# Performance work log

Measured on AMD Instinct MI355X. Metric: run time of the kernel, lower is better.

The kernel has to match this reference:

```python
import jax, jax.numpy as jnp
import numpy as np

B, N, D, H = 64, 197, 768, 12
HD = D // H          # 64
MLP = 4 * D          # 3072
WIN = 14
NUM_REL = (2 * WIN - 1) * (2 * WIN - 1) + 3  # 732
SCALE = HD ** -0.5
DCF_SCALE = 1.0
EPS = 1e-5


def _make_rel_index(wh, ww):
    coords = np.stack(np.meshgrid(np.arange(wh), np.arange(ww), indexing='ij'))  # [2, wh, ww]
    flat = coords.reshape(2, -1)
    rel = flat[:, :, None] - flat[:, None, :]          # [2, L, L]
    rel = rel.transpose(1, 2, 0).astype(np.int64)      # [L, L, 2]
    rel[..., 0] += wh - 1
    rel[..., 1] += ww - 1
    rel[..., 0] *= 2 * ww - 1
    idx = np.zeros((wh * ww + 1, wh * ww + 1), dtype=np.int32)
    idx[1:, 1:] = rel.sum(-1)
    nrd = (2 * wh - 1) * (2 * ww - 1) + 3
    idx[0, :] = nrd - 3
    idx[:, 0] = nrd - 2
    idx[0, 0] = nrd - 1
    return idx


def _ln(x, w, b):
    m = x.mean(-1, keepdims=True)
    v = ((x - m) ** 2).mean(-1, keepdims=True)
    return (x - m) * jax.lax.rsqrt(v + EPS) * w + b


def setup_inputs() -> dict:
    key = jax.random.key(0)
    ks = jax.random.split(key, 32)
    rnd = lambda i, shp, s=0.02: jax.random.normal(ks[i], shp, jnp.float32) * s
    return {
        'x': jax.random.normal(ks[0], (B, N, D), jnp.float32),
        'w_qkv': rnd(1, (3 * D, D)),
        'q_bias': rnd(2, (D,)),
        'v_bias': rnd(3, (D,)),
        'ssf_scale_qkv': 1.0 + rnd(4, (3 * D,)),
        'ssf_shift_qkv': rnd(5, (3 * D,)),
        'rel_bias_table': rnd(6, (NUM_REL, H)),
        'bases_coeff': rnd(7, (H, H)),
        'w_proj': rnd(8, (D, D)),
        'b_proj': rnd(9, (D,)),
        'ssf_scale_proj': 1.0 + rnd(10, (D,)),
        'ssf_shift_proj': rnd(11, (D,)),
        'norm1_w': jnp.ones((D,), jnp.float32),
        'norm1_b': jnp.zeros((D,), jnp.float32),
        'norm2_w': jnp.ones((D,), jnp.float32),
        'norm2_b': jnp.zeros((D,), jnp.float32),
        'ssf_scale_1': 1.0 + rnd(12, (D,)),
        'ssf_shift_1': rnd(13, (D,)),
        'ssf_scale_2': 1.0 + rnd(14, (D,)),
        'ssf_shift_2': rnd(15, (D,)),
        'w_fc1': rnd(16, (MLP, D)),
        'b_fc1': rnd(17, (MLP,)),
        'w_fc2': rnd(18, (D, MLP)),
        'b_fc2': rnd(19, (D,)),
        'ssf_scale_mlp': 1.0 + rnd(20, (D,)),
        'ssf_shift_mlp': rnd(21, (D,)),
        'gamma_1': jnp.full((D,), 0.1, jnp.float32),
        'gamma_2': jnp.full((D,), 0.1, jnp.float32),
        'rel_pos_index': jnp.asarray(_make_rel_index(WIN, WIN)),
    }


def reference(x, w_qkv, q_bias, v_bias, ssf_scale_qkv, ssf_shift_qkv,
              rel_bias_table, bases_coeff, w_proj, b_proj,
              ssf_scale_proj, ssf_shift_proj, norm1_w, norm1_b, norm2_w, norm2_b,
              ssf_scale_1, ssf_shift_1, ssf_scale_2, ssf_shift_2,
              w_fc1, b_fc1, w_fc2, b_fc2, ssf_scale_mlp, ssf_shift_mlp,
              gamma_1, gamma_2, rel_pos_index):
    # --- attention branch (eval mode: all dropouts are identity) ---
    h = _ln(x, norm1_w, norm1_b) * ssf_scale_1 + ssf_shift_1
    qkv_bias = jnp.concatenate([q_bias, jnp.zeros_like(v_bias), v_bias])
    qkv = h @ w_qkv.T + qkv_bias                       # [B, N, 3D]
    qkv = qkv * ssf_scale_qkv + ssf_shift_qkv
    qkv = qkv.reshape(B, N, 3, H, HD).transpose(2, 0, 3, 1, 4)  # [3, B, H, N, hd]
    q, k, v = qkv[0] * SCALE, qkv[1], qkv[2]
    attn = jnp.einsum('bhnd,bhmd->bhnm', q, k)         # [B, H, N, N]
    bias = rel_bias_table[rel_pos_index.reshape(-1)].reshape(N, N, H).transpose(2, 0, 1)
    attn = jax.nn.softmax(attn + bias[None], axis=-1)
    # dcf head mixing
    coeff = bases_coeff.T * DCF_SCALE + jnp.eye(H, dtype=attn.dtype)
    attn = jnp.einsum('bhnl,hk->bknl', attn, coeff)
    y = jnp.einsum('bhnm,bhmd->bnhd', attn, v).reshape(B, N, D)
    y = y @ w_proj.T + b_proj
    y = y * ssf_scale_proj + ssf_shift_proj
    x = x + gamma_1 * y
    # --- MLP branch ---
    h = _ln(x, norm2_w, norm2_b) * ssf_scale_2 + ssf_shift_2
    m = jax.nn.gelu(h @ w_fc1.T + b_fc1, approximate=False)
    m = m @ w_fc2.T + b_fc2
    m = m * ssf_scale_mlp + ssf_shift_mlp
    return x + gamma_2 * m
```

## Files before the change

### kernel.cpp

```cpp
#include <hip/hip_runtime.h>

typedef unsigned short u16;
using f32x4  = __attribute__((ext_vector_type(4))) float;
using bf16x8 = __attribute__((ext_vector_type(8))) __bf16;

#define Bz   64
#define Nn   197
#define Dd   768
#define Hh   12
#define HDp  64
#define MLPD 3072
#define ROWS (Bz*Nn)
#define NM   (Nn*Nn)
#define NPAD 224

#define OFF_H    0UL
#define OFF_X1   19365888UL
#define OFF_BIA  58097664UL
#define OFF_WB   59960496UL
#define OFF_CH   74116272UL
#define WQKV_E 0UL
#define WPRJ_E 1769472UL
#define WFC1_E 2359296UL
#define WFC2_E 4718592UL
#define QKV_B  907776UL
#define P_B    1059072UL
#define VT_B   344064UL
#define CHUNK_B 2310912UL

__device__ inline float b2f(u16 v){ unsigned u = ((unsigned)v) << 16; float f; __builtin_memcpy(&f,&u,4); return f; }
__device__ inline u16 f2b(float f){ unsigned u; __builtin_memcpy(&u,&f,4); u += 0x7FFFu + ((u>>16)&1u); return (u16)(u>>16); }

__device__ inline float gelu_f(float x){
    float z  = fabsf(x) * 0.70710678118f;
    float t  = 1.f / (1.f + 0.3275911f * z);
    float y  = t*(0.254829592f + t*(-0.284496736f + t*(1.421413741f + t*(-1.453152027f + t*1.061405429f))));
    float er = 1.f - y * __expf(-z*z);
    er = copysignf(er, x);
    return 0.5f * x * (1.f + er);
}

__device__ inline void gload_lds16(const u16* g, u16* l) {
    __builtin_amdgcn_global_load_lds((const __attribute__((address_space(1))) void*)g,
                                     (__attribute__((address_space(3))) void*)l, 16, 0, 0);
}

__global__ __launch_bounds__(256)
void conv_b16(const float* __restrict__ src, u16* __restrict__ dst, int n4)
{
    int t = blockIdx.x*256 + threadIdx.x;
    if (t >= n4) return;
    float4 v = *(const float4*)(src + (size_t)t*4);
    u16* d = dst + (size_t)t*4;
    d[0] = f2b(v.x); d[1] = f2b(v.y); d[2] = f2b(v.z); d[3] = f2b(v.w);
}

template<int EPI>
__global__ __launch_bounds__(512, 1)
void gemm256v(const u16* __restrict__ A, const u16* __restrict__ W, void* __restrict__ Cp,
              int M, int N, int K, int lda, int ldw,
              const float* __restrict__ e0, const float* __restrict__ e1,
              const float* __restrict__ e2, const float* __restrict__ e3,
              const float* __restrict__ ef)
{
    extern __shared__ u16 lds[];
    constexpr int SWEEP = 4096;
    constexpr int ICA  = 2;
    constexpr int ICB  = 2;
    constexpr int ASZ  = 256 * 32;
    constexpr int BSZ  = 256 * 32;
    constexpr int ABUF = 2 * ASZ;
    constexpr int BBUF = 2 * BSZ;
    constexpr int MF   = 8;
    constexpr int MH   = 4;

    u16* sA = lds;
    u16* sB = lds + 2 * ABUF;

    const int tid  = threadIdx.x;
    const int lane = tid & 63;
    const int wave = tid >> 6;
    const int wr   = wave >> 2;
    const int wc   = wave & 3;
    const int rid  = lane & 15;
    const int kg   = lane >> 4;
    const int m0   = blockIdx.y * 256;
    const int n0   = blockIdx.x * 256;
    const int t8   = tid * 8;

    const u16* asrc[2][ICA]; int adst[2][ICA];
    const u16* bsrc[2][ICB]; int bdst[2][ICB];
#pragma unroll
    for (int s = 0; s < 2; ++s) {
#pragma unroll
        for (int i = 0; i < ICA; ++i) {
            int e = i*SWEEP + t8, r = e >> 5;
            int g = ((e >> 3) & 3) ^ ((r >> 1) & 3);
            int row = m0 + r; if (row > M-1) row = M-1;
            asrc[s][i] = A + (size_t)row*lda + s*32 + g*8;
            adst[s][i] = s*ASZ + e;
        }
#pragma unroll
        for (int i = 0; i < ICB; ++i) {
            int e = i*SWEEP + t8, r = e >> 5;
            int g = ((e >> 3) & 3) ^ ((r >> 1) & 3);
            int col = n0 + r; if (col > N-1) col = N-1;
            bsrc[s][i] = W + (size_t)col*ldw + s*32 + g*8;
            bdst[s][i] = s*BSZ + e;
        }
    }

    const int koA   = (kg ^ ((rid >> 1) & 3)) * 8;
    const int aRow0 = (wr*128 + rid) * 32 + koA;
    const int bRow  = (wc*64  + rid) * 32 + koA;

    f32x4 acc[MF][4];
#pragma unroll
    for (int i = 0; i < MF; ++i)
#pragma unroll
        for (int j = 0; j < 4; ++j) acc[i][j] = (f32x4){0.f,0.f,0.f,0.f};

#pragma unroll
    for (int i = 0; i < ICA; ++i) gload_lds16(asrc[0][i], sA + adst[0][i]);
#pragma unroll
    for (int i = 0; i < ICB; ++i) gload_lds16(bsrc[0][i], sB + bdst[0][i]);
    asm volatile("" ::: "memory");
#pragma unroll
    for (int i = 0; i < ICA; ++i) gload_lds16(asrc[1][i], sA + adst[1][i]);
#pragma unroll
    for (int i = 0; i < ICB; ++i) gload_lds16(bsrc[1][i], sB + bdst[1][i]);

    const int NT = K >> 6;
    for (int t = 0; t < NT; ++t) {
        const int p  = t & 1;
        const size_t kpre = (size_t)(t + 1) * 64;
        const u16* paB = sA + p * ABUF;
        const u16* pbB = sB + p * BBUF;
        const int  qa  = (p ^ 1) * ABUF;
        const int  qb  = (p ^ 1) * BBUF;
        bf16x8 af[MH], wf[4];

        asm volatile("s_waitcnt vmcnt(4) lgkmcnt(0)\n\ts_barrier" ::: "memory");
#pragma unroll
        for (int i = 0; i < ICA; ++i) gload_lds16(asrc[0][i] + kpre, sA + adst[0][i] + qa);
#pragma unroll
        for (int i = 0; i < ICB; ++i) gload_lds16(bsrc[0][i] + kpre, sB + bdst[0][i] + qb);
        asm volatile("" ::: "memory");
#pragma unroll
        for (int i = 0; i < ICA; ++i) gload_lds16(asrc[1][i] + kpre, sA + adst[1][i] + qa);
#pragma unroll
        for (int i = 0; i < ICB; ++i) gload_lds16(bsrc[1][i] + kpre, sB + bdst[1][i] + qb);

        {
            const u16* pa = paB + aRow0;
#pragma unroll
            for (int f = 0; f < MH; ++f) af[f] = *(const bf16x8*)(pa + f*512);
            const u16* pb = pbB + bRow;
#pragma unroll
            for (int j = 0; j < 4; ++j) wf[j] = *(const bf16x8*)(pb + j*512);
            __builtin_amdgcn_s_setprio(1);
#pragma unroll
            for (int f = 0; f < MH; ++f)
#pragma unroll
                for (int j = 0; j < 4; ++j)
                    acc[f][j] = __builtin_amdgcn_mfma_f32_16x16x32_bf16(af[f], wf[j], acc[f][j], 0, 0, 0);
            __builtin_amdgcn_s_setprio(0);
        }
        {
            const u16* pa = paB + aRow0 + MH*512;
#pragma unroll
            for (int f = 0; f < MH; ++f) af[f] = *(const bf16x8*)(pa + f*512);
            __builtin_amdgcn_s_setprio(1);
#pragma unroll
            for (int f = 0; f < MH; ++f)
#pragma unroll
                for (int j = 0; j < 4; ++j)
                    acc[MH+f][j] = __builtin_amdgcn_mfma_f32_16x16x32_bf16(af[f], wf[j], acc[MH+f][j], 0, 0, 0);
            __builtin_amdgcn_s_setprio(0);
        }
        asm volatile("s_waitcnt vmcnt(8) lgkmcnt(0)\n\ts_barrier" ::: "memory");
        {
            const u16* pa = paB + ASZ + aRow0;
#pragma unroll
            for (int f = 0; f < MH; ++f) af[f] = *(const bf16x8*)(pa + f*512);
            const u16* pb = pbB + BSZ + bRow;
#pragma unroll
            for (int j = 0; j < 4; ++j) wf[j] = *(const bf16x8*)(pb + j*512);
            __builtin_amdgcn_s_setprio(1);
#pragma unroll
            for (int f = 0; f < MH; ++f)
#pragma unroll
                for (int j = 0; j < 4; ++j)
                    acc[f][j] = __builtin_amdgcn_mfma_f32_16x16x32_bf16(af[f], wf[j], acc[f][j], 0, 0, 0);
            __builtin_amdgcn_s_setprio(0);
        }
        {
            const u16* pa = paB + ASZ + aRow0 + MH*512;
#pragma unroll
            for (int f = 0; f < MH; ++f) af[f] = *(const bf16x8*)(pa + f*512);
            __builtin_amdgcn_s_setprio(1);
#pragma unroll
            for (int f = 0; f < MH; ++f)
#pragma unroll
                for (int j = 0; j < 4; ++j)
                    acc[MH+f][j] = __builtin_amdgcn_mfma_f32_16x16x32_bf16(af[f], wf[j], acc[MH+f][j], 0, 0, 0);
            __builtin_amdgcn_s_setprio(0);
        }
    }
    asm volatile("s_waitcnt vmcnt(0)" ::: "memory");
    __syncthreads();

    float* ka = (float*)lds;
    float* kb = ka + 256;
    if (tid < 256) {
        int gn = n0 + tid;
        if constexpr (EPI == 0) {
            float mql = (gn < 768) ? 0.125f : 1.f;
            float bias = 0.f;
            if (gn < 768) bias = e0[gn];
            else if (gn >= 1536) bias = e1[gn-1536];
            float sc = e2[gn];
            ka[tid] = sc * mql;
            kb[tid] = (bias * sc + e3[gn]) * mql;
        } else if constexpr (EPI == 4) {
            ka[tid] = 0.f;
            kb[tid] = e0[gn];
        } else {
            float sc = e1[gn];
            ka[tid] = sc;
            kb[tid] = e0[gn]*sc + e2[gn];
        }
    }
    __syncthreads();
    const int rq = (lane >> 4) * 4;
    const int cc = lane & 15;
    float kaj[4], kbj[4];
#pragma unroll
    for (int j = 0; j < 4; ++j) {
        int c = wc*64 + j*16 + cc;
        kaj[j] = ka[c]; kbj[j] = kb[c];
    }
    __syncthreads();

    if constexpr (EPI == 0 || EPI == 4) {
        u16* ct = lds;
#pragma unroll
        for (int i = 0; i < MF; ++i) {
#pragma unroll
            for (int j = 0; j < 4; ++j) {
#pragma unroll
                for (int r = 0; r < 4; ++r) {
                    int rowL = wr*128 + i*16 + rq + r;
                    int col  = wc*64 + j*16 + cc;
                    float v = acc[i][j][r];
                    u16 o;
                    if constexpr (EPI == 0) o = f2b(v*kaj[j] + kbj[j]);
                    else                    o = f2b(gelu_f(v + kbj[j]));
                    ct[rowL*264 + col] = o;
                }
            }
        }
        __syncthreads();
        constexpr int ldc = (EPI == 0) ? 2304 : 3072;
        u16* C = (u16*)Cp;
#pragma unroll
        for (int sw = 0; sw < 16; ++sw) {
            int rowL = sw*16 + (tid >> 5);
            int gm = m0 + rowL;
            if (gm < M) {
                int col0 = (tid & 31) * 8;
                *(uint4*)(C + (size_t)gm*ldc + n0 + col0) =
                    *(const uint4*)(ct + rowL*264 + col0);
            }
        }
    } else {
        float* cf = (float*)lds;
        float* C = (float*)Cp;
#pragma unroll
        for (int h = 0; h < 2; ++h) {
            if (wr == h) {
#pragma unroll
                for (int i = 0; i < MF; ++i) {
#pragma unroll
                    for (int j = 0; j < 4; ++j) {
#pragma unroll
                        for (int r = 0; r < 4; ++r) {
                            int rowH = i*16 + rq + r;
                            int col  = wc*64 + j*16 + cc;
                            cf[rowH*260 + col] = acc[i][j][r]*kaj[j] + kbj[j];
                        }
                    }
                }
            }
            __syncthreads();
#pragma unroll
            for (int sw = 0; sw < 16; ++sw) {
                int rowH = sw*8 + (tid >> 6);
                int gm = m0 + h*128 + rowH;
                if (gm < M) {
                    int col0 = (tid & 63) * 4;
                    f32x4 v  = *(const f32x4*)(cf + rowH*260 + col0);
                    size_t gidx = (size_t)gm*768 + n0 + col0;
                    f32x4 xv = *(const f32x4*)(ef + gidx);
                    f32x4 g3 = *(const f32x4*)(e3 + n0 + col0);
                    f32x4 o;
#pragma unroll
                    for (int q = 0; q < 4; ++q) o[q] = xv[q] + g3[q]*v[q];
                    *(f32x4*)(C + gidx) = o;
                }
            }
            __syncthreads();
        }
    }
}

template<int EPI>
__global__ __launch_bounds__(256, 2)
void gemm128p(const u16* __restrict__ A, const u16* __restrict__ W, void* __restrict__ Cp,
              int M, int N, int K, int lda, int ldw,
              const float* __restrict__ e0, const float* __restrict__ e1,
              const float* __restrict__ e2, const float* __restrict__ e3,
              const float* __restrict__ e4, const float* __restrict__ ef)
{
    extern __shared__ u16 lds[];
    constexpr int SWEEP = 2048;
    constexpr int ICA  = 2;
    constexpr int ICB  = 2;
    constexpr int ASZ  = 128 * 32;
    constexpr int BSZ  = 128 * 32;
    constexpr int ABUF = 2 * ASZ;
    constexpr int BBUF = 2 * BSZ;
    constexpr int MF   = 4;
    constexpr int MH   = 2;

    u16* sA = lds;
    u16* sB = lds + 2 * ABUF;

    const int tid  = threadIdx.x;
    const int lane = tid & 63;
    const int wave = tid >> 6;
    const int wr   = wave >> 1;
    const int wc   = wave & 1;
    const int rid  = lane & 15;
    const int kg   = lane >> 4;
    const int m0   = blockIdx.y * 128;
    const int n0   = blockIdx.x * 128;
    const int t8   = tid * 8;

    const u16* asrc[2][ICA]; int adst[2][ICA];
    const u16* bsrc[2][ICB]; int bdst[2][ICB];
#pragma unroll
    for (int s = 0; s < 2; ++s) {
#pragma unroll
        for (int i = 0; i < ICA; ++i) {
            int e = i*SWEEP + t8, r = e >> 5;
            int g = ((e >> 3) & 3) ^ ((r >> 1) & 3);
            int row = m0 + r; if (row > M-1) row = M-1;
            asrc[s][i] = A + (size_t)row*lda + s*32 + g*8;
            adst[s][i] = s*ASZ + e;
        }
#pragma unroll
        for (int i = 0; i < ICB; ++i) {
            int e = i*SWEEP + t8, r = e >> 5;
            int g = ((e >> 3) & 3) ^ ((r >> 1) & 3);
            int col = n0 + r; if (col > N-1) col = N-1;
            bsrc[s][i] = W + (size_t)col*ldw + s*32 + g*8;
            bdst[s][i] = s*BSZ + e;
        }
    }

    const int koA   = (kg ^ ((rid >> 1) & 3)) * 8;
    const int aRow0 = (wr*64 + rid) * 32 + koA;
    const int bRow  = (wc*64 + rid) * 32 + koA;

    f32x4 acc[MF][4];
#pragma unroll
    for (int i = 0; i < MF; ++i)
#pragma unroll
        for (int j = 0; j < 4; ++j) acc[i][j] = (f32x4){0.f,0.f,0.f,0.f};

#pragma unroll
    for (int i = 0; i < ICA; ++i) gload_lds16(asrc[0][i], sA + adst[0][i]);
#pragma unroll
    for (int i = 0; i < ICB; ++i) gload_lds16(bsrc[0][i], sB + bdst[0][i]);
    asm volatile("" ::: "memory");
#pragma unroll
    for (int i = 0; i < ICA; ++i) gload_lds16(asrc[1][i], sA + adst[1][i]);
#pragma unroll
    for (int i = 0; i < ICB; ++i) gload_lds16(bsrc[1][i], sB + bdst[1][i]);

    const int NT = K >> 6;
    for (int t = 0; t < NT; ++t) {
        const int p  = t & 1;
        const size_t kpre = (size_t)(t + 1) * 64;
        const u16* paB = sA + p * ABUF;
        const u16* pbB = sB + p * BBUF;
        const int  qa  = (p ^ 1) * ABUF;
        const int  qb  = (p ^ 1) * BBUF;
        bf16x8 af[MH], wf[4];

        asm volatile("s_waitcnt vmcnt(4) lgkmcnt(0)\n\ts_barrier" ::: "memory");
#pragma unroll
        for (int i = 0; i < ICA; ++i) gload_lds16(asrc[0][i] + kpre, sA + adst[0][i] + qa);
#pragma unroll
        for (int i = 0; i < ICB; ++i) gload_lds16(bsrc[0][i] + kpre, sB + bdst[0][i] + qb);
        asm volatile("" ::: "memory");
#pragma unroll
        for (int i = 0; i < ICA; ++i) gload_lds16(asrc[1][i] + kpre, sA + adst[1][i] + qa);
#pragma unroll
        for (int i = 0; i < ICB; ++i) gload_lds16(bsrc[1][i] + kpre, sB + bdst[1][i] + qb);

        {
            const u16* pa = paB + aRow0;
#pragma unroll
            for (int f = 0; f < MH; ++f) af[f] = *(const bf16x8*)(pa + f*512);
            const u16* pb = pbB + bRow;
#pragma unroll
            for (int j = 0; j < 4; ++j) wf[j] = *(const bf16x8*)(pb + j*512);
            __builtin_amdgcn_s_setprio(1);
#pragma unroll
            for (int f = 0; f < MH; ++f)
#pragma unroll
                for (int j = 0; j < 4; ++j)
                    acc[f][j] = __builtin_amdgcn_mfma_f32_16x16x32_bf16(af[f], wf[j], acc[f][j], 0, 0, 0);
            __builtin_amdgcn_s_setprio(0);
        }
        {
            const u16* pa = paB + aRow0 + MH*512;
#pragma unroll
            for (int f = 0; f < MH; ++f) af[f] = *(const bf16x8*)(pa + f*512);
            __builtin_amdgcn_s_setprio(1);
#pragma unroll
            for (int f = 0; f < MH; ++f)
#pragma unroll
                for (int j = 0; j < 4; ++j)
                    acc[MH+f][j] = __builtin_amdgcn_mfma_f32_16x16x32_bf16(af[f], wf[j], acc[MH+f][j], 0, 0, 0);
            __builtin_amdgcn_s_setprio(0);
        }
        asm volatile("s_waitcnt vmcnt(8) lgkmcnt(0)\n\ts_barrier" ::: "memory");
        {
            const u16* pa = paB + ASZ + aRow0;
#pragma unroll
            for (int f = 0; f < MH; ++f) af[f] = *(const bf16x8*)(pa + f*512);
            const u16* pb = pbB + BSZ + bRow;
#pragma unroll
            for (int j = 0; j < 4; ++j) wf[j] = *(const bf16x8*)(pb + j*512);
            __builtin_amdgcn_s_setprio(1);
#pragma unroll
            for (int f = 0; f < MH; ++f)
#pragma unroll
                for (int j = 0; j < 4; ++j)
                    acc[f][j] = __builtin_amdgcn_mfma_f32_16x16x32_bf16(af[f], wf[j], acc[f][j], 0, 0, 0);
            __builtin_amdgcn_s_setprio(0);
        }
        {
            const u16* pa = paB + ASZ + aRow0 + MH*512;
#pragma unroll
            for (int f = 0; f < MH; ++f) af[f] = *(const bf16x8*)(pa + f*512);
            __builtin_amdgcn_s_setprio(1);
#pragma unroll
            for (int f = 0; f < MH; ++f)
#pragma unroll
                for (int j = 0; j < 4; ++j)
                    acc[MH+f][j] = __builtin_amdgcn_mfma_f32_16x16x32_bf16(af[f], wf[j], acc[MH+f][j], 0, 0, 0);
            __builtin_amdgcn_s_setprio(0);
        }
    }
    asm volatile("s_waitcnt vmcnt(0)" ::: "memory");
    __syncthreads();

    float* ka = (float*)lds;
    float* kb = ka + 128;
    if (tid < 128) {
        int gn = n0 + tid;
        float sc = e1[gn];
        ka[tid] = sc;
        kb[tid] = e0[gn]*sc + e2[gn];
    }
    __syncthreads();
    const int rq = (lane >> 4) * 4;
    const int cc = lane & 15;
    float kaj[4], kbj[4];
#pragma unroll
    for (int j = 0; j < 4; ++j) {
        int c = wc*64 + j*16 + cc;
        kaj[j] = ka[c]; kbj[j] = kb[c];
    }
    __syncthreads();

    float* cf = (float*)lds;
    const float* RES = e4;
    float* C = (float*)Cp;
#pragma unroll
    for (int h = 0; h < 2; ++h) {
        if (wr == h) {
#pragma unroll
            for (int i = 0; i < MF; ++i) {
#pragma unroll
                for (int j = 0; j < 4; ++j) {
#pragma unroll
                    for (int r = 0; r < 4; ++r) {
                        int rowH = i*16 + rq + r;
                        int col  = wc*64 + j*16 + cc;
                        cf[rowH*132 + col] = acc[i][j][r]*kaj[j] + kbj[j];
                    }
                }
            }
        }
        __syncthreads();
#pragma unroll
        for (int sw = 0; sw < 8; ++sw) {
            int rowH = sw*8 + (tid >> 5);
            int gm = m0 + h*64 + rowH;
            if (gm < M) {
                int col0 = (tid & 31) * 4;
                f32x4 v  = *(const f32x4*)(cf + rowH*132 + col0);
                size_t gidx = (size_t)gm*768 + n0 + col0;
                f32x4 xv = *(const f32x4*)(RES + gidx);
                f32x4 g3 = *(const f32x4*)(e3 + n0 + col0);
                f32x4 o;
#pragma unroll
                for (int q = 0; q < 4; ++q) o[q] = xv[q] + g3[q]*v[q];
                *(f32x4*)(C + gidx) = o;
            }
        }
        __syncthreads();
    }
}

template<int EPI>
__global__ __launch_bounds__(256)
void gemm_nt(const u16* __restrict__ A, const u16* __restrict__ W, void* __restrict__ Cp,
             int M, int N, int K, int lda, int ldw, int b0,
             const float* __restrict__ ef)
{
    __shared__ __align__(16) u16 csm[(EPI == 1) ? 32768 : 16384];
    const int tid  = threadIdx.x;
    const int lane = tid & 63;
    const int wave = tid >> 6;
    const int z    = blockIdx.z;
    const int m0   = wave*64;
    const int n0   = blockIdx.x*64;
    const int rid  = lane & 15;
    const int kq   = (lane >> 4) * 8;

    const u16* Ab = A;
    const u16* Wb = W;
    if constexpr (EPI == 1) {
        int bb = z/12, hh = z - bb*12;
        Ab = A + ((size_t)bb*Nn)*2304 + hh*64;
        Wb = W + ((size_t)bb*Nn)*2304 + 768 + hh*64;
    } else {
        Ab = A + (size_t)z*Nn*NPAD;
        Wb = W + (size_t)z*HDp*NPAD;
    }

    f32x4 acc[4][4];
#pragma unroll
    for (int i = 0; i < 4; ++i)
#pragma unroll
        for (int j = 0; j < 4; ++j) acc[i][j] = (f32x4){0.f,0.f,0.f,0.f};

    for (int k0 = 0; k0 < K; k0 += 32) {
        bf16x8 af[4], wf[4];
#pragma unroll
        for (int i = 0; i < 4; ++i) {
            int r = m0 + i*16 + rid; if (r > M-1) r = M-1;
            af[i] = *(const bf16x8*)(Ab + (size_t)r*lda + k0 + kq);
        }
#pragma unroll
        for (int j = 0; j < 4; ++j) {
            int c = n0 + j*16 + rid; if (c > N-1) c = N-1;
            wf[j] = *(const bf16x8*)(Wb + (size_t)c*ldw + k0 + kq);
        }
#pragma unroll
        for (int i = 0; i < 4; ++i)
#pragma unroll
            for (int j = 0; j < 4; ++j)
                acc[i][j] = __builtin_amdgcn_mfma_f32_16x16x32_bf16(af[i], wf[j], acc[i][j], 0, 0, 0);
    }

    const int rq = (lane >> 4) * 4;
    const int cc = lane & 15;

    if constexpr (EPI == 1) {
        float* cs = (float*)csm;
#pragma unroll
        for (int i = 0; i < 4; ++i)
#pragma unroll
            for (int j = 0; j < 4; ++j)
#pragma unroll
                for (int r = 0; r < 4; ++r)
                    cs[(m0 + i*16 + rq + r)*64 + j*16 + cc] = acc[i][j][r];
        __syncthreads();
        int hh = z - (z/12)*12;
        const float* bsrc = ef + (size_t)hh*NM;
        u16* P = (u16*)Cp + (size_t)z*Nn*NPAD;
        for (int sw = 0; sw < 13; ++sw) {
            int row = sw*16 + (tid >> 4);
            int col0 = (tid & 15) * 4;
            int gn = n0 + col0;
            if (row < Nn && gn < NPAD) {
                f32x4 v = *(const f32x4*)(cs + row*64 + col0);
                const float* bp = bsrc + (size_t)row*Nn + gn;
                float b0v = bp[0], b1v = bp[1], b2v = bp[2], b3v = bp[3];
                unsigned lo = (unsigned)f2b(v[0]+b0v) | ((unsigned)f2b(v[1]+b1v) << 16);
                unsigned hi = (unsigned)f2b(v[2]+b2v) | ((unsigned)f2b(v[3]+b3v) << 16);
                uint2 pk; pk.x = lo; pk.y = hi;
                *(uint2*)(P + (size_t)row*NPAD + gn) = pk;
            }
        }
    } else {
        u16* cs = csm;
#pragma unroll
        for (int i = 0; i < 4; ++i)
#pragma unroll
            for (int j = 0; j < 4; ++j)
#pragma unroll
                for (int r = 0; r < 4; ++r)
                    cs[(m0 + i*16 + rq + r)*64 + j*16 + cc] = f2b(acc[i][j][r]);
        __syncthreads();
        int bb = z/12, kk = z - bb*12;
        u16* Y = (u16*)Cp + ((size_t)(b0+bb)*Nn)*768 + kk*64;
        for (int sw = 0; sw < 7; ++sw) {
            int row = sw*32 + (tid >> 3);
            if (row < Nn) {
                int col0 = (tid & 7) * 8;
                *(uint4*)(Y + (size_t)row*768 + col0) = *(const uint4*)(cs + row*64 + col0);
            }
        }
    }
}

__global__ __launch_bounds__(256)
void ln_ssf(const float* __restrict__ x, const float* __restrict__ w, const float* __restrict__ bb,
            const float* __restrict__ sc, const float* __restrict__ sh, u16* __restrict__ out)
{
    const int row = blockIdx.x, tid = threadIdx.x;
    const float* xr = x + (size_t)row * 768;
    float v[3], s1 = 0.f, s2 = 0.f;
#pragma unroll
    for (int i = 0; i < 3; ++i) {
        float f = xr[tid + i*256];
        v[i] = f; s1 += f; s2 += f*f;
    }
    for (int o = 32; o > 0; o >>= 1) { s1 += __shfl_xor(s1, o); s2 += __shfl_xor(s2, o); }
    __shared__ float r1[4], r2[4];
    int wv = tid >> 6;
    if ((tid & 63) == 0) { r1[wv] = s1; r2[wv] = s2; }
    __syncthreads();
    s1 = r1[0]+r1[1]+r1[2]+r1[3];
    s2 = r2[0]+r2[1]+r2[2]+r2[3];
    float mean = s1 * (1.f/768.f);
    float var  = s2 * (1.f/768.f) - mean*mean;
    float rstd = rsqrtf(fmaxf(var, 0.f) + 1e-5f);
#pragma unroll
    for (int i = 0; i < 3; ++i) {
        int c = tid + i*256;
        float h = (v[i] - mean) * rstd * w[c] + bb[c];
        h = h * sc[c] + sh[c];
        out[(size_t)row*768 + c] = f2b(h);
    }
}

__global__ __launch_bounds__(256)
void bias_gather(const int* __restrict__ idx, const float* __restrict__ table, float* __restrict__ biasf)
{
    int t = blockIdx.x*256 + threadIdx.x;
    if (t >= NM) return;
    int id = idx[t];
#pragma unroll
    for (int h = 0; h < 12; ++h)
        biasf[(size_t)h*NM + t] = table[id*12 + h];
}

__global__ __launch_bounds__(256)
void softmax_dcf(u16* __restrict__ P, const float* __restrict__ bases, int nb)
{
    __shared__ float cf[144];
    int tid = threadIdx.x;
    if (tid < 144) {
        int k = tid / 12, h = tid - k*12;
        cf[h*12 + k] = bases[k*12 + h] + (h == k ? 1.f : 0.f);
    }
    __syncthreads();
    int ridx = blockIdx.x*4 + (tid >> 6);
    if (ridx >= nb*Nn) return;
    int lane = tid & 63;
    int m0 = lane * 4;
    int bb = ridx / Nn, n = ridx - bb*Nn;
    const size_t hs = (size_t)Nn*NPAD;
    u16* base = P + ((size_t)bb*12)*hs + (size_t)n*NPAD;

    float e[12][4];
#pragma unroll
    for (int h = 0; h < 12; ++h) {
        float s[4];
        if (m0 < NPAD) {
            uint2 pv = *(const uint2*)(base + h*hs + m0);
            s[0] = b2f((u16)(pv.x & 0xFFFF)); s[1] = b2f((u16)(pv.x >> 16));
            s[2] = b2f((u16)(pv.y & 0xFFFF)); s[3] = b2f((u16)(pv.y >> 16));
        } else { s[0]=s[1]=s[2]=s[3] = -1e30f; }
#pragma unroll
        for (int j = 0; j < 4; ++j) if (m0 + j >= Nn) s[j] = -1e30f;
        float mx = fmaxf(fmaxf(s[0], s[1]), fmaxf(s[2], s[3]));
        for (int o = 32; o > 0; o >>= 1) mx = fmaxf(mx, __shfl_xor(mx, o));
        float sum = 0.f;
#pragma unroll
        for (int j = 0; j < 4; ++j) {
            float ev = __expf(fmaxf(s[j] - mx, -80.f));
            if (m0 + j >= Nn) ev = 0.f;
            e[h][j] = ev; sum += ev;
        }
        for (int o = 32; o > 0; o >>= 1) sum += __shfl_xor(sum, o);
        float inv = 1.f / sum;
#pragma unroll
        for (int j = 0; j < 4; ++j) e[h][j] *= inv;
    }
    if (m0 < NPAD) {
#pragma unroll
        for (int k = 0; k < 12; ++k) {
            float o0 = 0.f, o1 = 0.f, o2 = 0.f, o3 = 0.f;
#pragma unroll
            for (int h = 0; h < 12; ++h) {
                float c = cf[h*12 + k];
                o0 += e[h][0]*c; o1 += e[h][1]*c; o2 += e[h][2]*c; o3 += e[h][3]*c;
            }
            unsigned lo = (unsigned)f2b(o0) | ((unsigned)f2b(o1) << 16);
            unsigned hi = (unsigned)f2b(o2) | ((unsigned)f2b(o3) << 16);
            uint2 pk; pk.x = lo; pk.y = hi;
            *(uint2*)(base + k*hs + m0) = pk;
        }
    }
}

__global__ __launch_bounds__(256)
void v_transpose(const u16* __restrict__ qkv, u16* __restrict__ vT)
{
    __shared__ u16 lds[64*198];
    int z = blockIdx.x;
    int bb = z/12, hh = z - bb*12;
    int tid = threadIdx.x;
    const u16* src = qkv + ((size_t)bb*Nn)*2304 + 1536 + hh*64;
    for (int e = tid; e < Nn*64; e += 256) {
        int m = e >> 6, d = e & 63;
        lds[d*198 + m] = src[(size_t)m*2304 + d];
    }
    __syncthreads();
    u16* dst = vT + (size_t)z*64*NPAD;
    for (int e = tid; e < 64*NPAD; e += 256) {
        int d = e / NPAD, m = e - d*NPAD;
        dst[e] = (m < Nn) ? lds[d*198 + m] : (u16)0;
    }
}

extern "C" void kernel_launch(void* const* d_in, const int* in_sizes, int n_in,
                              void* d_out, int out_size, void* d_ws, size_t ws_size,
                              hipStream_t stream)
{
    const float* x       = (const float*)d_in[0];
    const float* w_qkv   = (const float*)d_in[1];
    const float* q_bias  = (const float*)d_in[2];
    const float* v_bias  = (const float*)d_in[3];
    const float* s_qkv   = (const float*)d_in[4];
    const float* sh_qkv  = (const float*)d_in[5];
    const float* rel_tab = (const float*)d_in[6];
    const float* bases   = (const float*)d_in[7];
    const float* w_proj  = (const float*)d_in[8];
    const float* b_proj  = (const float*)d_in[9];
    const float* s_proj  = (const float*)d_in[10];
    const float* sh_proj = (const float*)d_in[11];
    const float* n1w     = (const float*)d_in[12];
    const float* n1b     = (const float*)d_in[13];
    const float* n2w     = (const float*)d_in[14];
    const float* n2b     = (const float*)d_in[15];
    const float* ss1     = (const float*)d_in[16];
    const float* ssh1    = (const float*)d_in[17];
    const float* ss2     = (const float*)d_in[18];
    const float* ssh2    = (const float*)d_in[19];
    const float* w_fc1   = (const float*)d_in[20];
    const float* b_fc1   = (const float*)d_in[21];
    const float* w_fc2   = (const float*)d_in[22];
    const float* b_fc2   = (const float*)d_in[23];
    const float* s_mlp   = (const float*)d_in[24];
    const float* sh_mlp  = (const float*)d_in[25];
    const float* g1      = (const float*)d_in[26];
    const float* g2      = (const float*)d_in[27];
    const int*   relidx  = (const int*)d_in[28];

    char*  ws   = (char*)d_ws;
    u16*   hbuf = (u16*)(ws + OFF_H);
    float* x1   = (float*)(ws + OFF_X1);
    float* bia  = (float*)(ws + OFF_BIA);
    u16*   wb   = (u16*)(ws + OFF_WB);
    float* out  = (float*)d_out;

    u16* wqkvB = wb + WQKV_E;
    u16* wprjB = wb + WPRJ_E;
    u16* wfc1B = wb + WFC1_E;
    u16* wfc2B = wb + WFC2_E;

    hipFuncSetAttribute(reinterpret_cast<const void*>(&gemm256v<0>),
                        hipFuncAttributeMaxDynamicSharedMemorySize, 139264);
    hipFuncSetAttribute(reinterpret_cast<const void*>(&gemm256v<4>),
                        hipFuncAttributeMaxDynamicSharedMemorySize, 139264);
    hipFuncSetAttribute(reinterpret_cast<const void*>(&gemm256v<5>),
                        hipFuncAttributeMaxDynamicSharedMemorySize, 139264);
    hipFuncSetAttribute(reinterpret_cast<const void*>(&gemm128p<3>),
                        hipFuncAttributeMaxDynamicSharedMemorySize, 65536);

    int nb = 64;
    while (nb > 1 && OFF_CH + (size_t)nb*CHUNK_B > ws_size) nb >>= 1;
    const int nchunk = 64 / nb;
    u16* qkvC = (u16*)(ws + OFF_CH);
    u16* PC   = (u16*)(ws + OFF_CH + (size_t)nb*QKV_B);
    u16* vTC  = (u16*)(ws + OFF_CH + (size_t)nb*(QKV_B + P_B));

    conv_b16<<<dim3(1728), dim3(256), 0, stream>>>(w_qkv, wqkvB, 442368);
    conv_b16<<<dim3(576),  dim3(256), 0, stream>>>(w_proj, wprjB, 147456);
    conv_b16<<<dim3(2304), dim3(256), 0, stream>>>(w_fc1, wfc1B, 589824);
    conv_b16<<<dim3(2304), dim3(256), 0, stream>>>(w_fc2, wfc2B, 589824);

    ln_ssf<<<dim3(ROWS), dim3(256), 0, stream>>>(x, n1w, n1b, ss1, ssh1, hbuf);
    bias_gather<<<dim3(152), dim3(256), 0, stream>>>(relidx, rel_tab, bia);

    for (int c = 0; c < nchunk; ++c) {
        const int b0 = c * nb;
        const int nrows = nb * Nn;
        const int gy = (nrows + 255) / 256;
        gemm256v<0><<<dim3(9, gy), dim3(512), 139264, stream>>>(
            hbuf + (size_t)b0*Nn*768, wqkvB, qkvC,
            nrows, 2304, 768, 768, 768, q_bias, v_bias, s_qkv, sh_qkv, nullptr);
        v_transpose<<<dim3(nb*12), dim3(256), 0, stream>>>(qkvC, vTC);
        gemm_nt<1><<<dim3(4, 1, nb*12), dim3(256), 0, stream>>>(
            qkvC, qkvC, PC, Nn, Nn, 64, 2304, 2304, 0, bia);
        softmax_dcf<<<dim3((nb*Nn + 3)/4), dim3(256), 0, stream>>>(PC, bases, nb);
        gemm_nt<2><<<dim3(1, 1, nb*12), dim3(256), 0, stream>>>(
            PC, vTC, hbuf, Nn, 64, NPAD, NPAD, NPAD, b0, nullptr);
    }

    gemm128p<3><<<dim3(6, 99), dim3(256), 65536, stream>>>(
        hbuf, wprjB, x1, ROWS, 768, 768, 768, 768,
        b_proj, s_proj, sh_proj, g1, x, nullptr);
    ln_ssf<<<dim3(ROWS), dim3(256), 0, stream>>>(x1, n2w, n2b, ss2, ssh2, hbuf);

    u16* mlpC = qkvC;
    size_t avail = (ws_size > OFF_CH) ? (ws_size - OFF_CH) : (size_t)CHUNK_B;
    int nrM = (int)(avail / (MLPD * 2));
    if (nrM < 1) nrM = 1;
    if (nrM > ROWS) nrM = ROWS;
    for (int r0 = 0; r0 < ROWS; r0 += nrM) {
        int cr = ROWS - r0; if (cr > nrM) cr = nrM;
        int gy = (cr + 255) / 256;
        gemm256v<4><<<dim3(12, gy), dim3(512), 139264, stream>>>(
            hbuf + (size_t)r0*768, wfc1B, mlpC, cr, 3072, 768, 768, 768,
            b_fc1, nullptr, nullptr, nullptr, nullptr);
        gemm256v<5><<<dim3(3, gy), dim3(512), 139264, stream>>>(
            mlpC, wfc2B, out + (size_t)r0*768, cr, 768, 3072, 3072, 3072,
            b_fc2, s_mlp, sh_mlp, g2, x1 + (size_t)r0*768);
    }
}
```

Before: 744.8 us.

## Generalize big GEMM to 16 waves, interleave prefetch loads with MFMA phases

Templates the 256-row GEMM on tile width and thread count, and runs QKV and FC1 with 1024 threads so each wave owns a 64x64 sub-tile instead of 128x64. FC2 now uses a 256x128 tile with 512 threads, doubling its grid width for better CU coverage. The global-to-LDS prefetches are split and interleaved between the MFMA sub-phases rather than issued all at once at the top of each iteration, with the waitcnt/barrier thresholds adjusted to match. The smaller per-wave tiles lower register use and raise the wave count per CU. The cost is less data reuse per wave and more barrier participants per block.

```diff
diff --git a/kernel.cpp b/kernel.cpp
--- a/kernel.cpp
+++ b/kernel.cpp
@@ -55,24 +55,27 @@
     d[0] = f2b(v.x); d[1] = f2b(v.y); d[2] = f2b(v.z); d[3] = f2b(v.w);
 }
 
-template<int EPI>
-__global__ __launch_bounds__(512, 1)
-void gemm256v(const u16* __restrict__ A, const u16* __restrict__ W, void* __restrict__ Cp,
-              int M, int N, int K, int lda, int ldw,
-              const float* __restrict__ e0, const float* __restrict__ e1,
-              const float* __restrict__ e2, const float* __restrict__ e3,
-              const float* __restrict__ ef)
+template<int EPI, int BN, int TH>
+__global__ __launch_bounds__(TH)
+void gemmv(const u16* __restrict__ A, const u16* __restrict__ W, void* __restrict__ Cp,
+           int M, int N, int K, int lda, int ldw,
+           const float* __restrict__ e0, const float* __restrict__ e1,
+           const float* __restrict__ e2, const float* __restrict__ e3,
+           const float* __restrict__ ef)
 {
     extern __shared__ u16 lds[];
-    constexpr int SWEEP = 4096;
-    constexpr int ICA  = 2;
-    constexpr int ICB  = 2;
-    constexpr int ASZ  = 256 * 32;
-    constexpr int BSZ  = 256 * 32;
+    constexpr int BM   = 256;
+    constexpr int SWEEP = TH * 8;
+    constexpr int ICA  = (BM * 32) / SWEEP;
+    constexpr int ICB  = (BN * 32) / SWEEP;
+    constexpr int VN   = ICA + ICB;
+    constexpr int ASZ  = BM * 32;
+    constexpr int BSZ  = BN * 32;
     constexpr int ABUF = 2 * ASZ;
     constexpr int BBUF = 2 * BSZ;
-    constexpr int MF   = 8;
-    constexpr int MH   = 4;
+    constexpr int WCN  = BN / 64;
+    constexpr int MF   = 4;
+    constexpr int MH   = 2;
 
     u16* sA = lds;
     u16* sB = lds + 2 * ABUF;
@@ -80,12 +83,12 @@
     const int tid  = threadIdx.x;
     const int lane = tid & 63;
     const int wave = tid >> 6;
-    const int wr   = wave >> 2;
-    const int wc   = wave & 3;
+    const int wr   = wave / WCN;
+    const int wc   = wave % WCN;
     const int rid  = lane & 15;
     const int kg   = lane >> 4;
-    const int m0   = blockIdx.y * 256;
-    const int n0   = blockIdx.x * 256;
+    const int m0   = blockIdx.y * BM;
+    const int n0   = blockIdx.x * BN;
     const int t8   = tid * 8;
 
     const u16* asrc[2][ICA]; int adst[2][ICA];
@@ -111,14 +114,20 @@
     }
 
     const int koA   = (kg ^ ((rid >> 1) & 3)) * 8;
-    const int aRow0 = (wr*128 + rid) * 32 + koA;
-    const int bRow  = (wc*64  + rid) * 32 + koA;
+    const int aRow0 = (wr*64 + rid) * 32 + koA;
+    const int bRow  = (wc*64 + rid) * 32 + koA;
 
     f32x4 acc[MF][4];
 #pragma unroll
     for (int i = 0; i < MF; ++i)
 #pragma unroll
         for (int j = 0; j < 4; ++j) acc[i][j] = (f32x4){0.f,0.f,0.f,0.f};
+
+#define WAITBAR() do { \
+        if constexpr (VN == 2)      asm volatile("s_waitcnt vmcnt(2) lgkmcnt(0)\n\ts_barrier" ::: "memory"); \
+        else if constexpr (VN == 3) asm volatile("s_waitcnt vmcnt(3) lgkmcnt(0)\n\ts_barrier" ::: "memory"); \
+        else                        asm volatile("s_waitcnt vmcnt(4) lgkmcnt(0)\n\ts_barrier" ::: "memory"); \
+    } while (0)
 
 #pragma unroll
     for (int i = 0; i < ICA; ++i) gload_lds16(asrc[0][i], sA + adst[0][i]);
@@ -129,6 +138,7 @@
     for (int i = 0; i < ICA; ++i) gload_lds16(asrc[1][i], sA + adst[1][i]);
 #pragma unroll
     for (int i = 0; i < ICB; ++i) gload_lds16(bsrc[1][i], sB + bdst[1][i]);
+    WAITBAR();
 
     const int NT = K >> 6;
     for (int t = 0; t < NT; ++t) {
@@ -140,17 +150,6 @@
         const int  qb  = (p ^ 1) * BBUF;
         bf16x8 af[MH], wf[4];
 
-        asm volatile("s_waitcnt vmcnt(4) lgkmcnt(0)\n\ts_barrier" ::: "memory");
-#pragma unroll
-        for (int i = 0; i < ICA; ++i) gload_lds16(asrc[0][i] + kpre, sA + adst[0][i] + qa);
-#pragma unroll
-        for (int i = 0; i < ICB; ++i) gload_lds16(bsrc[0][i] + kpre, sB + bdst[0][i] + qb);
-        asm volatile("" ::: "memory");
-#pragma unroll
-        for (int i = 0; i < ICA; ++i) gload_lds16(asrc[1][i] + kpre, sA + adst[1][i] + qa);
-#pragma unroll
-        for (int i = 0; i < ICB; ++i) gload_lds16(bsrc[1][i] + kpre, sB + bdst[1][i] + qb);
-
         {
             const u16* pa = paB + aRow0;
 #pragma unroll
@@ -158,6 +157,8 @@
             const u16* pb = pbB + bRow;
 #pragma unroll
             for (int j = 0; j < 4; ++j) wf[j] = *(const bf16x8*)(pb + j*512);
+#pragma unroll
+            for (int i = 0; i < ICA; ++i) gload_lds16(asrc[0][i] + kpre, sA + adst[0][i] + qa);
             __builtin_amdgcn_s_setprio(1);
 #pragma unroll
             for (int f = 0; f < MH; ++f)
@@ -170,6 +171,8 @@
             const u16* pa = paB + aRow0 + MH*512;
 #pragma unroll
             for (int f = 0; f < MH; ++f) af[f] = *(const bf16x8*)(pa + f*512);
+#pragma unroll
+            for (int i = 0; i < ICB; ++i) gload_lds16(bsrc[0][i] + kpre, sB + bdst[0][i] + qb);
             __builtin_amdgcn_s_setprio(1);
 #pragma unroll
             for (int f = 0; f < MH; ++f)
@@ -178,7 +181,7 @@
                     acc[MH+f][j] = __builtin_amdgcn_mfma_f32_16x16x32_bf16(af[f], wf[j], acc[MH+f][j], 0, 0, 0);
             __builtin_amdgcn_s_setprio(0);
         }
-        asm volatile("s_waitcnt vmcnt(8) lgkmcnt(0)\n\ts_barrier" ::: "memory");
+        WAITBAR();
         {
             const u16* pa = paB + ASZ + aRow0;
 #pragma unroll
@@ -186,6 +189,8 @@
             const u16* pb = pbB + BSZ + bRow;
 #pragma unroll
             for (int j = 0; j < 4; ++j) wf[j] = *(const bf16x8*)(pb + j*512);
+#pragma unroll
+            for (int i = 0; i < ICA; ++i) gload_lds16(asrc[1][i] + kpre, sA + adst[1][i] + qa);
             __builtin_amdgcn_s_setprio(1);
 #pragma unroll
             for (int f = 0; f < MH; ++f)
@@ -198,6 +203,8 @@
             const u16* pa = paB + ASZ + aRow0 + MH*512;
 #pragma unroll
             for (int f = 0; f < MH; ++f) af[f] = *(const bf16x8*)(pa + f*512);
+#pragma unroll
+            for (int i = 0; i < ICB; ++i) gload_lds16(bsrc[1][i] + kpre, sB + bdst[1][i] + qb);
             __builtin_amdgcn_s_setprio(1);
 #pragma unroll
             for (int f = 0; f < MH; ++f)
@@ -206,13 +213,15 @@
                     acc[MH+f][j] = __builtin_amdgcn_mfma_f32_16x16x32_bf16(af[f], wf[j], acc[MH+f][j], 0, 0, 0);
             __builtin_amdgcn_s_setprio(0);
         }
+        WAITBAR();
     }
     asm volatile("s_waitcnt vmcnt(0)" ::: "memory");
     __syncthreads();
+#undef WAITBAR
 
     float* ka = (float*)lds;
-    float* kb = ka + 256;
-    if (tid < 256) {
+    float* kb = ka + BN;
+    if (tid < BN) {
         int gn = n0 + tid;
         if constexpr (EPI == 0) {
             float mql = (gn < 768) ? 0.125f : 1.f;
@@ -250,7 +259,7 @@
             for (int j = 0; j < 4; ++j) {
 #pragma unroll
                 for (int r = 0; r < 4; ++r) {
-                    int rowL = wr*128 + i*16 + rq + r;
+                    int rowL = wr*64 + i*16 + rq + r;
                     int col  = wc*64 + j*16 + cc;
                     float v = acc[i][j][r];
                     u16 o;
@@ -263,9 +272,10 @@
         __syncthreads();
         constexpr int ldc = (EPI == 0) ? 2304 : 3072;
         u16* C = (u16*)Cp;
-#pragma unroll
-        for (int sw = 0; sw < 16; ++sw) {
-            int rowL = sw*16 + (tid >> 5);
+        constexpr int RPS = TH / 32;
+#pragma unroll
+        for (int sw = 0; sw < 256/RPS; ++sw) {
+            int rowL = sw*RPS + (tid >> 5);
             int gm = m0 + rowL;
             if (gm < M) {
                 int col0 = (tid & 31) * 8;
@@ -278,28 +288,28 @@
         float* C = (float*)Cp;
 #pragma unroll
         for (int h = 0; h < 2; ++h) {
-            if (wr == h) {
+            if ((wr >> 1) == h) {
 #pragma unroll
                 for (int i = 0; i < MF; ++i) {
 #pragma unroll
                     for (int j = 0; j < 4; ++j) {
 #pragma unroll
                         for (int r = 0; r < 4; ++r) {
-                            int rowH = i*16 + rq + r;
+                            int rowH = (wr & 1)*64 + i*16 + rq + r;
                             int col  = wc*64 + j*16 + cc;
-                            cf[rowH*260 + col] = acc[i][j][r]*kaj[j] + kbj[j];
+                            cf[rowH*132 + col] = acc[i][j][r]*kaj[j] + kbj[j];
                         }
                     }
                 }
             }
             __syncthreads();
 #pragma unroll
-            for (int sw = 0; sw < 16; ++sw) {
-                int rowH = sw*8 + (tid >> 6);
+            for (int sw = 0; sw < 8; ++sw) {
+                int rowH = sw*16 + (tid >> 5);
                 int gm = m0 + h*128 + rowH;
                 if (gm < M) {
-                    int col0 = (tid & 63) * 4;
-                    f32x4 v  = *(const f32x4*)(cf + rowH*260 + col0);
+                    int col0 = (tid & 31) * 4;
+                    f32x4 v  = *(const f32x4*)(cf + rowH*132 + col0);
                     size_t gidx = (size_t)gm*768 + n0 + col0;
                     f32x4 xv = *(const f32x4*)(ef + gidx);
                     f32x4 g3 = *(const f32x4*)(e3 + n0 + col0);
@@ -379,6 +389,8 @@
 #pragma unroll
         for (int j = 0; j < 4; ++j) acc[i][j] = (f32x4){0.f,0.f,0.f,0.f};
 
+#define WAITBAR() asm volatile("s_waitcnt vmcnt(4) lgkmcnt(0)\n\ts_barrier" ::: "memory")
+
 #pragma unroll
     for (int i = 0; i < ICA; ++i) gload_lds16(asrc[0][i], sA + adst[0][i]);
 #pragma unroll
@@ -388,6 +400,7 @@
     for (int i = 0; i < ICA; ++i) gload_lds16(asrc[1][i], sA + adst[1][i]);
 #pragma unroll
     for (int i = 0; i < ICB; ++i) gload_lds16(bsrc[1][i], sB + bdst[1][i]);
+    WAITBAR();
 
     const int NT = K >> 6;
     for (int t = 0; t < NT; ++t) {
@@ -399,17 +412,6 @@
         const int  qb  = (p ^ 1) * BBUF;
         bf16x8 af[MH], wf[4];
 
-        asm volatile("s_waitcnt vmcnt(4) lgkmcnt(0)\n\ts_barrier" ::: "memory");
-#pragma unroll
-        for (int i = 0; i < ICA; ++i) gload_lds16(asrc[0][i] + kpre, sA + adst[0][i] + qa);
-#pragma unroll
-        for (int i = 0; i < ICB; ++i) gload_lds16(bsrc[0][i] + kpre, sB + bdst[0][i] + qb);
-        asm volatile("" ::: "memory");
-#pragma unroll
-        for (int i = 0; i < ICA; ++i) gload_lds16(asrc[1][i] + kpre, sA + adst[1][i] + qa);
-#pragma unroll
-        for (int i = 0; i < ICB; ++i) gload_lds16(bsrc[1][i] + kpre, sB + bdst[1][i] + qb);
-
         {
             const u16* pa = paB + aRow0;
 #pragma unroll
@@ -417,6 +419,8 @@
             const u16* pb = pbB + bRow;
 #pragma unroll
             for (int j = 0; j < 4; ++j) wf[j] = *(const bf16x8*)(pb + j*512);
+#pragma unroll
+            for (int i = 0; i < ICA; ++i) gload_lds16(asrc[0][i] + kpre, sA + adst[0][i] + qa);
             __builtin_amdgcn_s_setprio(1);
 #pragma unroll
             for (int f = 0; f < MH; ++f)
@@ -429,6 +433,8 @@
             const u16* pa = paB + aRow0 + MH*512;
 #pragma unroll
             for (int f = 0; f < MH; ++f) af[f] = *(const bf16x8*)(pa + f*512);
+#pragma unroll
+            for (int i = 0; i < ICB; ++i) gload_lds16(bsrc[0][i] + kpre, sB + bdst[0][i] + qb);
             __builtin_amdgcn_s_setprio(1);
 #pragma unroll
             for (int f = 0; f < MH; ++f)
@@ -437,7 +443,7 @@
                     acc[MH+f][j] = __builtin_amdgcn_mfma_f32_16x16x32_bf16(af[f], wf[j], acc[MH+f][j], 0, 0, 0);
             __builtin_amdgcn_s_setprio(0);
         }
-        asm volatile("s_waitcnt vmcnt(8) lgkmcnt(0)\n\ts_barrier" ::: "memory");
+        WAITBAR();
         {
             const u16* pa = paB + ASZ + aRow0;
 #pragma unroll
@@ -445,6 +451,8 @@
             const u16* pb = pbB + BSZ + bRow;
 #pragma unroll
             for (int j = 0; j < 4; ++j) wf[j] = *(const bf16x8*)(pb + j*512);
+#pragma unroll
+            for (int i = 0; i < ICA; ++i) gload_lds16(asrc[1][i] + kpre, sA + adst[1][i] + qa);
             __builtin_amdgcn_s_setprio(1);
 #pragma unroll
             for (int f = 0; f < MH; ++f)
@@ -457,6 +465,8 @@
             const u16* pa = paB + ASZ + aRow0 + MH*512;
 #pragma unroll
             for (int f = 0; f < MH; ++f) af[f] = *(const bf16x8*)(pa + f*512);
+#pragma unroll
+            for (int i = 0; i < ICB; ++i) gload_lds16(bsrc[1][i] + kpre, sB + bdst[1][i] + qb);
             __builtin_amdgcn_s_setprio(1);
 #pragma unroll
             for (int f = 0; f < MH; ++f)
@@ -465,9 +475,11 @@
                     acc[MH+f][j] = __builtin_amdgcn_mfma_f32_16x16x32_bf16(af[f], wf[j], acc[MH+f][j], 0, 0, 0);
             __builtin_amdgcn_s_setprio(0);
         }
+        WAITBAR();
     }
     asm volatile("s_waitcnt vmcnt(0)" ::: "memory");
     __syncthreads();
+#undef WAITBAR
 
     float* ka = (float*)lds;
     float* kb = ka + 128;
@@ -800,12 +812,12 @@
     u16* wfc1B = wb + WFC1_E;
     u16* wfc2B = wb + WFC2_E;
 
-    hipFuncSetAttribute(reinterpret_cast<const void*>(&gemm256v<0>),
+    hipFuncSetAttribute(reinterpret_cast<const void*>(&gemmv<0,256,1024>),
                         hipFuncAttributeMaxDynamicSharedMemorySize, 139264);
-    hipFuncSetAttribute(reinterpret_cast<const void*>(&gemm256v<4>),
+    hipFuncSetAttribute(reinterpret_cast<const void*>(&gemmv<4,256,1024>),
                         hipFuncAttributeMaxDynamicSharedMemorySize, 139264);
-    hipFuncSetAttribute(reinterpret_cast<const void*>(&gemm256v<5>),
-                        hipFuncAttributeMaxDynamicSharedMemorySize, 139264);
+    hipFuncSetAttribute(reinterpret_cast<const void*>(&gemmv<5,128,512>),
+                        hipFuncAttributeMaxDynamicSharedMemorySize, 98304);
     hipFuncSetAttribute(reinterpret_cast<const void*>(&gemm128p<3>),
                         hipFuncAttributeMaxDynamicSharedMemorySize, 65536);
 
@@ -828,7 +840,7 @@
         const int b0 = c * nb;
         const int nrows = nb * Nn;
         const int gy = (nrows + 255) / 256;
-        gemm256v<0><<<dim3(9, gy), dim3(512), 139264, stream>>>(
+        gemmv<0,256,1024><<<dim3(9, gy), dim3(1024), 139264, stream>>>(
             hbuf + (size_t)b0*Nn*768, wqkvB, qkvC,
             nrows, 2304, 768, 768, 768, q_bias, v_bias, s_qkv, sh_qkv, nullptr);
         v_transpose<<<dim3(nb*12), dim3(256), 0, stream>>>(qkvC, vTC);
@@ -852,10 +864,10 @@
     for (int r0 = 0; r0 < ROWS; r0 += nrM) {
         int cr = ROWS - r0; if (cr > nrM) cr = nrM;
         int gy = (cr + 255) / 256;
-        gemm256v<4><<<dim3(12, gy), dim3(512), 139264, stream>>>(
+        gemmv<4,256,1024><<<dim3(12, gy), dim3(1024), 139264, stream>>>(
             hbuf + (size_t)r0*768, wfc1B, mlpC, cr, 3072, 768, 768, 768,
             b_fc1, nullptr, nullptr, nullptr, nullptr);
-        gemm256v<5><<<dim3(3, gy), dim3(512), 139264, stream>>>(
+        gemmv<5,128,512><<<dim3(6, gy), dim3(512), 98304, stream>>>(
             mlpC, wfc2B, out + (size_t)r0*768, cr, 768, 3072, 3072, 3072,
             b_fc2, s_mlp, sh_mlp, g2, x1 + (size_t)r0*768);
     }
```

Measured after the change: 715.9 us. 3.9% less time.
